# Performance work log

Hardware: AMD Instinct MI355X
Metric: run time of the kernel (lower is better)

## Reference

```python
import jax, jax.numpy as jnp
import numpy as np
import math

D_MODEL = 2048
NUM_HEADS = 16
HEAD_DIM = D_MODEL // NUM_HEADS  # 128
B, S = 2, 2048


def setup_inputs() -> dict:
    key = jax.random.key(0)
    ks = jax.random.split(key, 11)
    s_in = 1.0 / math.sqrt(D_MODEL)
    return {
        "query": jax.random.normal(ks[0], (B, S, D_MODEL), dtype=jnp.float32),
        "key": jax.random.normal(ks[1], (B, S, D_MODEL), dtype=jnp.float32),
        "value": jax.random.normal(ks[2], (B, S, D_MODEL), dtype=jnp.float32),
        "Wq": jax.random.normal(ks[3], (D_MODEL, D_MODEL), dtype=jnp.float32) * s_in,
        "bq": jnp.zeros((D_MODEL,), dtype=jnp.float32),
        "Wk": jax.random.normal(ks[4], (D_MODEL, HEAD_DIM), dtype=jnp.float32) * s_in,
        "bk": jnp.zeros((HEAD_DIM,), dtype=jnp.float32),
        "Wv": jax.random.normal(ks[5], (D_MODEL, HEAD_DIM), dtype=jnp.float32) * s_in,
        "bv": jnp.zeros((HEAD_DIM,), dtype=jnp.float32),
        "Wo": jax.random.normal(ks[6], (D_MODEL, D_MODEL), dtype=jnp.float32) * s_in,
        "bo": jnp.zeros((D_MODEL,), dtype=jnp.float32),
    }


def reference(query, key, value, Wq, bq, Wk, bk, Wv, bv, Wo, bo):
    b, s, d_model = query.shape
    h, d = NUM_HEADS, HEAD_DIM
    # Projections: Q has h heads, K/V have a single shared head (MQA)
    Q = (query @ Wq + bq).reshape(b, s, h, d).transpose(0, 2, 1, 3)  # [b,h,s,d]
    K = key @ Wk + bk      # [b,s,d]
    V = value @ Wv + bv    # [b,s,d]
    scale = 1.0 / math.sqrt(d)
    # broadcast single K head over all h query heads
    scores = jnp.einsum('bhqd,bkd->bhqk', Q, K) * scale  # [b,h,s,s]
    weights = jax.nn.softmax(scores, axis=-1)
    attn = jnp.einsum('bhqk,bkd->bhqd', weights, V)      # [b,h,s,d]
    attn = attn.transpose(0, 2, 1, 3).reshape(b, s, d_model)
    return attn @ Wo + bo
```

## Files before the change

### kernel.cpp

```cpp
#include <hip/hip_runtime.h>


typedef unsigned short u16;
typedef __attribute__((ext_vector_type(8))) short bf16x8;
typedef __attribute__((ext_vector_type(4))) short bf16x4;
typedef __attribute__((ext_vector_type(4))) float f32x4;

#define D_MODEL 2048
#define SEQ     2048
#define NH      16
#define HD      128
#define BK      32

__device__ __forceinline__ u16 f2bf(float f){
  union { float f; unsigned u; } v; v.f = f;
  unsigned r = (v.u + 0x7FFFu + ((v.u >> 16) & 1u)) >> 16;
  return (u16)r;
}

#if __has_builtin(__builtin_amdgcn_cvt_pk_bf16_f32)
__device__ __forceinline__ unsigned pack2bf(float a, float b){
  auto v = __builtin_amdgcn_cvt_pk_bf16_f32(a, b);
  unsigned u; __builtin_memcpy(&u, &v, 4); return u;
}
#else
__device__ __forceinline__ unsigned pack2bf(float a, float b){
  return (unsigned)f2bf(a) | ((unsigned)f2bf(b) << 16);
}
#endif

__device__ __forceinline__ void gll16(const void* g, void* l){
  __builtin_amdgcn_global_load_lds(
      (const __attribute__((address_space(1))) void*)g,
      (__attribute__((address_space(3))) void*)l, 16, 0, 0);
}

__global__ __launch_bounds__(256) void convert3_kernel(
    const float4* __restrict__ a, const float4* __restrict__ b, const float4* __restrict__ c,
    ushort4* __restrict__ oa, ushort4* __restrict__ ob, ushort4* __restrict__ oc){
  int i = blockIdx.x*256 + threadIdx.x;
  float4 va = a[i], vb = b[i], vc = c[i];
  ushort4 ra, rb, rc;
  ra.x=f2bf(va.x); ra.y=f2bf(va.y); ra.z=f2bf(va.z); ra.w=f2bf(va.w);
  rb.x=f2bf(vb.x); rb.y=f2bf(vb.y); rb.z=f2bf(vb.z); rb.w=f2bf(vb.w);
  rc.x=f2bf(vc.x); rc.y=f2bf(vc.y); rc.z=f2bf(vc.z); rc.w=f2bf(vc.w);
  oa[i]=ra; ob[i]=rb; oc[i]=rc;
}

__global__ __launch_bounds__(256) void transpose_all(
    const float* __restrict__ Wq, const float* __restrict__ Wo,
    const float* __restrict__ Wk, const float* __restrict__ Wv,
    u16* __restrict__ WqT, u16* __restrict__ WoT,
    u16* __restrict__ WkT, u16* __restrict__ WvT){
  __shared__ float tt[32][33];
  int id = blockIdx.x;
  const float* in; u16* outp; int C, bx, by;
  if (id < 4096)      { in=Wq; outp=WqT; C=2048; bx=id&63;        by=id>>6; }
  else if (id < 8192) { id-=4096; in=Wo; outp=WoT; C=2048; bx=id&63; by=id>>6; }
  else if (id < 8448) { id-=8192; in=Wk; outp=WkT; C=128;  bx=id&3;  by=id>>2; }
  else                { id-=8448; in=Wv; outp=WvT; C=128;  bx=id&3;  by=id>>2; }
  const int R = 2048;
  int c0 = bx*32, r0 = by*32;
  int tx = threadIdx.x & 31, ty = threadIdx.x >> 5;
  #pragma unroll
  for (int k=0;k<4;k++) tt[ty+k*8][tx] = in[(size_t)(r0+ty+k*8)*C + c0+tx];
  __syncthreads();
  #pragma unroll
  for (int k=0;k<4;k++) outp[(size_t)(c0+ty+k*8)*R + r0+tx] = f2bf(tt[tx][ty+k*8]);
}

__device__ __forceinline__ void gemm_core_db(
    const u16* __restrict__ A, const u16* __restrict__ BT,
    int lda, int ldb, int m0, int n0, int kbeg, int kend,
    u16* As, u16* Bs, f32x4 acc[4][4])
{
  const int t = threadIdx.x;
  const int w = t >> 6, l = t & 63;
  const int wr = w >> 1, wc = w & 1;
  const int c16 = l & 15, q = l >> 4;
  const int srow = l >> 2;
  const int sc   = ((l & 3) ^ ((l >> 3) & 3)) * 8;

  int aoff[4], boff[4];
  #pragma unroll
  for (int mt=0;mt<4;mt++){
    int row = wr*64 + mt*16 + c16;
    aoff[mt] = row*BK + ((q ^ ((row>>1)&3))*8);
  }
  #pragma unroll
  for (int nt=0;nt<4;nt++){
    int row = wc*64 + nt*16 + c16;
    boff[nt] = row*BK + ((q ^ ((row>>1)&3))*8);
  }

  auto issue = [&](int k0, int buf){
    u16* Ad = As + buf*4096;
    u16* Bd = Bs + buf*4096;
    #pragma unroll
    for (int half=0; half<2; half++){
      int r = half*64 + w*16 + srow;
      gll16(A  + (size_t)(m0+r)*lda + k0 + sc, Ad + (half*64 + w*16)*BK);
      gll16(BT + (size_t)(n0+r)*ldb + k0 + sc, Bd + (half*64 + w*16)*BK);
    }
  };

  const int n = (kend - kbeg) / BK;
  issue(kbeg, 0);
  for (int i = 0; i < n; i++){
    __syncthreads();
    if (i+1 < n) issue(kbeg + (i+1)*BK, (i+1)&1);
    const u16* Ab = As + (i&1)*4096;
    const u16* Bb = Bs + (i&1)*4096;
    bf16x8 af[4], bfr[4];
    #pragma unroll
    for (int mt=0;mt<4;mt++) af[mt]  = *(const bf16x8*)(Ab + aoff[mt]);
    #pragma unroll
    for (int nt=0;nt<4;nt++) bfr[nt] = *(const bf16x8*)(Bb + boff[nt]);
    #pragma unroll
    for (int mt=0;mt<4;mt++)
      #pragma unroll
      for (int nt=0;nt<4;nt++)
        acc[mt][nt] = __builtin_amdgcn_mfma_f32_16x16x32_bf16(af[mt], bfr[nt], acc[mt][nt], 0,0,0);
  }
}

__global__ __launch_bounds__(256) void proj_kernel(
    const u16* __restrict__ qb, const u16* __restrict__ kb, const u16* __restrict__ vb,
    const u16* __restrict__ WqT, const u16* __restrict__ WkT, const u16* __restrict__ WvT,
    const float* __restrict__ bq, u16* __restrict__ Qp, float* __restrict__ part)
{
  __shared__ u16 As[2*4096], Bs[2*4096];
  f32x4 acc[4][4];
  f32x4 z = {0.f,0.f,0.f,0.f};
  #pragma unroll
  for (int i=0;i<4;i++) for (int j=0;j<4;j++) acc[i][j] = z;
  const int t = threadIdx.x, w = t>>6, l = t&63, wr = w>>1, wc = w&1, c16 = l&15, q = l>>4;
  int id = blockIdx.x;
  if (id < 512){
    int m0 = (id & 31)*128, n0 = (id >> 5)*128;
    gemm_core_db(qb, WqT, 2048, 2048, m0, n0, 0, 2048, As, Bs, acc);
    #pragma unroll
    for (int mt=0;mt<4;mt++)
      #pragma unroll
      for (int nt=0;nt<4;nt++){
        int col = n0 + wc*64 + nt*16 + c16;
        float bv = bq[col];
        #pragma unroll
        for (int r=0;r<4;r++){
          int row = m0 + wr*64 + mt*16 + q*4 + r;
          Qp[(size_t)row*D_MODEL + col] = f2bf(acc[mt][nt][r] + bv);
        }
      }
  } else {
    int kvid = id - 512;
    int zi = kvid & 3, nb = (kvid >> 2) & 1, mi = kvid >> 3;
    const u16* Am = nb ? vb  : kb;
    const u16* Bm = nb ? WvT : WkT;
    gemm_core_db(Am, Bm, 2048, 2048, mi*128, 0, zi*512, zi*512+512, As, Bs, acc);
    float* dst = part + (size_t)(zi*2 + nb)*524288;
    #pragma unroll
    for (int mt=0;mt<4;mt++)
      #pragma unroll
      for (int nt=0;nt<4;nt++){
        int col = wc*64 + nt*16 + c16;
        #pragma unroll
        for (int r=0;r<4;r++){
          int row = mi*128 + wr*64 + mt*16 + q*4 + r;
          dst[(size_t)row*128 + col] = acc[mt][nt][r];
        }
      }
  }
}

__global__ __launch_bounds__(256) void oproj_kernel(
    const u16* __restrict__ A, const u16* __restrict__ BT, const float* __restrict__ bias,
    float* __restrict__ C)
{
  __shared__ u16 As[2*4096], Bs[2*4096];
  f32x4 acc[4][4];
  f32x4 z = {0.f,0.f,0.f,0.f};
  #pragma unroll
  for (int i=0;i<4;i++) for (int j=0;j<4;j++) acc[i][j] = z;
  int m0 = blockIdx.x*128, n0 = blockIdx.y*128;
  gemm_core_db(A, BT, 2048, 2048, m0, n0, 0, 2048, As, Bs, acc);
  const int t = threadIdx.x, w = t>>6, l = t&63, wr = w>>1, wc = w&1, c16 = l&15, q = l>>4;
  #pragma unroll
  for (int mt=0;mt<4;mt++)
    #pragma unroll
    for (int nt=0;nt<4;nt++){
      int col = n0 + wc*64 + nt*16 + c16;
      float bv = bias[col];
      #pragma unroll
      for (int r=0;r<4;r++){
        int row = m0 + wr*64 + mt*16 + q*4 + r;
        C[(size_t)row*D_MODEL + col] = acc[mt][nt][r] + bv;
      }
    }
}

__global__ __launch_bounds__(256) void kv_reduce_kernel(
    const float* __restrict__ part, const float* __restrict__ bk, const float* __restrict__ bv,
    u16* __restrict__ Kp, u16* __restrict__ VpT){
  int idx = blockIdx.x*256 + threadIdx.x;
  int d = idx & 127, sg = idx >> 7;
  float ka = 0.f, va = 0.f;
  #pragma unroll
  for (int zi=0; zi<4; zi++){
    ka += part[(size_t)(zi*2+0)*524288 + idx];
    va += part[(size_t)(zi*2+1)*524288 + idx];
  }
  Kp[idx] = f2bf(ka + bk[d]);
  int b = sg >> 11, sl = sg & 2047;
  VpT[(size_t)b*262144 + (size_t)d*2048 + sl] = f2bf(va + bv[d]);
}

__global__ __launch_bounds__(512, 4) void attn_kernel(
    const u16* __restrict__ Qp, const u16* __restrict__ Kp,
    const u16* __restrict__ VpT, u16* __restrict__ attnb){
  __shared__ u16 lds[32768];
  u16* Ks = lds;
  u16* Vs = lds + 16384;
  const int t = threadIdx.x;
  const int w = t >> 6, l = t & 63;
  const int c16 = l & 15, q = l >> 4;

  const int qt = blockIdx.x;
  const int bh = blockIdx.y;
  const int b = bh >> 4, h = bh & 15;

  const u16* Qbase = Qp  + ((size_t)(b*SEQ + qt*128 + w*16))*D_MODEL + h*HD;
  const u16* Kbase = Kp  + (size_t)(b*SEQ)*HD;
  const u16* Vbase = VpT + (size_t)b*HD*SEQ;

  {
    u16* qtmp = Vs + w*2048;
    #pragma unroll
    for (int j=0;j<4;j++){
      int r = j*4 + (l >> 4);
      int g = (l & 15) ^ (r & 15);
      gll16(Qbase + (size_t)r*D_MODEL + g*8, qtmp + j*512);
    }
  }
  #pragma unroll
  for (int j=0;j<4;j++){
    int r = j*32 + w*4 + (l >> 4);
    int g = (l & 15) ^ (r & 15);
    gll16(Kbase + (size_t)r*HD + g*8, Ks + j*4096 + w*512);
  }
  __syncthreads();
  bf16x8 qf[4];
  #pragma unroll
  for (int kk=0;kk<4;kk++){
    int ch = kk*4 + q;
    qf[kk] = *(const bf16x8*)(Vs + w*2048 + c16*128 + ((ch ^ c16) & 15)*8);
  }
  __syncthreads();

  f32x4 o[8];
  f32x4 z4 = {0.f,0.f,0.f,0.f};
  #pragma unroll
  for (int dt=0;dt<8;dt++) o[dt] = z4;
  float mrow = -1e30f, lrow = 0.f;
  const float cs = 0.08838834764831845f * 1.4426950408889634f;

  for (int kt = 0; kt < 16; kt++){
    #pragma unroll
    for (int j=0;j<4;j++){
      int d = j*32 + w*4 + (l >> 4);
      int g = (l & 15) ^ (d & 15);
      gll16(Vbase + (size_t)d*SEQ + kt*128 + g*8, Vs + j*4096 + w*512);
    }

    f32x4 s[8];
    #pragma unroll
    for (int kt8=0;kt8<8;kt8++) s[kt8] = z4;
    __builtin_amdgcn_s_setprio(1);
    #pragma unroll
    for (int kt8=0; kt8<8; kt8++){
      #pragma unroll
      for (int kk=0;kk<4;kk++){
        int ch = kk*4 + q;
        bf16x8 kf = *(const bf16x8*)(Ks + (kt8*16 + c16)*128 + ((ch ^ c16) & 15)*8);
        s[kt8] = __builtin_amdgcn_mfma_f32_16x16x32_bf16(kf, qf[kk], s[kt8], 0,0,0);
      }
    }
    __builtin_amdgcn_s_setprio(0);

    float x[8];
    #pragma unroll
    for (int kt8=0;kt8<8;kt8++)
      x[kt8] = fmaxf(fmaxf(s[kt8][0],s[kt8][1]), fmaxf(s[kt8][2],s[kt8][3]));
    float vmax = fmaxf(fmaxf(fmaxf(x[0],x[1]),fmaxf(x[2],x[3])),
                       fmaxf(fmaxf(x[4],x[5]),fmaxf(x[6],x[7])));
    vmax = fmaxf(vmax, __shfl_xor(vmax, 16));
    vmax = fmaxf(vmax, __shfl_xor(vmax, 32));
    float mnew = fmaxf(mrow, vmax);
    float alpha = exp2f((mrow - mnew)*cs);
    float mc = mnew*cs;
    float rs[8];
    #pragma unroll
    for (int kt8=0;kt8<8;kt8++){
      float p0 = exp2f(__builtin_fmaf(s[kt8][0], cs, -mc));
      float p1 = exp2f(__builtin_fmaf(s[kt8][1], cs, -mc));
      float p2 = exp2f(__builtin_fmaf(s[kt8][2], cs, -mc));
      float p3 = exp2f(__builtin_fmaf(s[kt8][3], cs, -mc));
      s[kt8][0]=p0; s[kt8][1]=p1; s[kt8][2]=p2; s[kt8][3]=p3;
      rs[kt8] = (p0+p1)+(p2+p3);
    }
    float rsum = ((rs[0]+rs[1])+(rs[2]+rs[3])) + ((rs[4]+rs[5])+(rs[6]+rs[7]));
    rsum += __shfl_xor(rsum, 16);
    rsum += __shfl_xor(rsum, 32);
    lrow = lrow*alpha + rsum;
    mrow = mnew;

    unsigned long long allone = __ballot(alpha == 1.f);
    if (allone != ~0ull){
      #pragma unroll
      for (int dt=0;dt<8;dt++)
        #pragma unroll
        for (int r=0;r<4;r++) o[dt][r] *= alpha;
    }

    union PU { unsigned u[4]; bf16x8 v; } P32[4];
    #pragma unroll
    for (int kb=0;kb<4;kb++){
      P32[kb].u[0] = pack2bf(s[2*kb][0],   s[2*kb][1]);
      P32[kb].u[1] = pack2bf(s[2*kb][2],   s[2*kb][3]);
      P32[kb].u[2] = pack2bf(s[2*kb+1][0], s[2*kb+1][1]);
      P32[kb].u[3] = pack2bf(s[2*kb+1][2], s[2*kb+1][3]);
    }

    __syncthreads();

    if (kt < 15){
      #pragma unroll
      for (int j=0;j<4;j++){
        int r = j*32 + w*4 + (l >> 4);
        int g = (l & 15) ^ (r & 15);
        gll16(Kbase + (size_t)((kt+1)*128 + r)*HD + g*8, Ks + j*4096 + w*512);
      }
    }

    __builtin_amdgcn_s_setprio(1);
    #pragma unroll
    for (int kb=0; kb<4; kb++){
      int ca = 4*kb + (q>>1);
      int cb = ca + 2;
      #pragma unroll
      for (int dt=0; dt<8; dt++){
        int d = dt*16 + c16;
        union VU { bf16x4 h[2]; bf16x8 v; } vf;
        vf.h[0] = *(const bf16x4*)(Vs + d*128 + ((ca ^ c16) & 15)*8 + (q&1)*4);
        vf.h[1] = *(const bf16x4*)(Vs + d*128 + ((cb ^ c16) & 15)*8 + (q&1)*4);
        o[dt] = __builtin_amdgcn_mfma_f32_16x16x32_bf16(vf.v, P32[kb].v, o[dt], 0,0,0);
      }
    }
    __builtin_amdgcn_s_setprio(0);
    __syncthreads();
  }

  float inv = 1.f / lrow;
  int qrow = qt*128 + w*16 + c16;
  u16* dst = attnb + ((size_t)(b*SEQ) + qrow)*D_MODEL + h*HD + q*4;
  #pragma unroll
  for (int dt=0;dt<8;dt++){
    ushort4 pk;
    pk.x = f2bf(o[dt][0]*inv);
    pk.y = f2bf(o[dt][1]*inv);
    pk.z = f2bf(o[dt][2]*inv);
    pk.w = f2bf(o[dt][3]*inv);
    *(ushort4*)(dst + dt*16) = pk;
  }
}

extern "C" void kernel_launch(void* const* d_in, const int* in_sizes, int n_in,
                              void* d_out, int out_size, void* d_ws, size_t ws_size,
                              hipStream_t stream) {
  (void)in_sizes; (void)n_in; (void)out_size; (void)ws_size;
  const float* query = (const float*)d_in[0];
  const float* key   = (const float*)d_in[1];
  const float* value = (const float*)d_in[2];
  const float* Wq    = (const float*)d_in[3];
  const float* bq    = (const float*)d_in[4];
  const float* Wk    = (const float*)d_in[5];
  const float* bk    = (const float*)d_in[6];
  const float* Wv    = (const float*)d_in[7];
  const float* bv    = (const float*)d_in[8];
  const float* Wo    = (const float*)d_in[9];
  const float* bo    = (const float*)d_in[10];
  float* out = (float*)d_out;

  char* W = (char*)d_ws;
  u16*  qb     = (u16*) (W + 0);
  u16*  kb     = (u16*) (W + 16777216);
  u16*  vb     = (u16*) (W + 33554432);
  u16*  WqT    = (u16*) (W + 50331648);
  u16*  WoT    = (u16*) (W + 58720256);
  u16*  WkT    = (u16*) (W + 67108864);
  u16*  WvT    = (u16*) (W + 67633152);
  u16*  Qp     = (u16*) (W + 68157440);
  u16*  Kp     = (u16*) (W + 84934656);
  u16*  VpT    = (u16*) (W + 85983232);
  u16*  attnb  = (u16*) (W + 87031808);
  float* kvpart= (float*)(W + 103809024);

  convert3_kernel<<<8192, 256, 0, stream>>>(
      (const float4*)query, (const float4*)key, (const float4*)value,
      (ushort4*)qb, (ushort4*)kb, (ushort4*)vb);
  transpose_all<<<8704, 256, 0, stream>>>(Wq, Wo, Wk, Wv, WqT, WoT, WkT, WvT);
  proj_kernel<<<768, 256, 0, stream>>>(qb, kb, vb, WqT, WkT, WvT, bq, Qp, kvpart);
  kv_reduce_kernel<<<2048, 256, 0, stream>>>(kvpart, bk, bv, Kp, VpT);
  attn_kernel<<<dim3(16,32), 512, 0, stream>>>(Qp, Kp, VpT, attnb);
  oproj_kernel<<<dim3(32,16), 256, 0, stream>>>(attnb, WoT, bo, out);
}
```

Before: 432.4 us.

## Process two query subtiles per wave to reuse K/V fragments in attention

Measured after the change: 410.6 us. -5.0%, faster.

```diff
diff --git a/kernel.cpp b/kernel.cpp
--- a/kernel.cpp
+++ b/kernel.cpp
@@ -214,7 +214,7 @@
   VpT[(size_t)b*262144 + (size_t)d*2048 + sl] = f2bf(va + bv[d]);
 }
 
-__global__ __launch_bounds__(512, 4) void attn_kernel(
+__global__ __launch_bounds__(512, 2) void attn_kernel(
     const u16* __restrict__ Qp, const u16* __restrict__ Kp,
     const u16* __restrict__ VpT, u16* __restrict__ attnb){
   __shared__ u16 lds[32768];
@@ -228,39 +228,30 @@
   const int bh = blockIdx.y;
   const int b = bh >> 4, h = bh & 15;
 
-  const u16* Qbase = Qp  + ((size_t)(b*SEQ + qt*128 + w*16))*D_MODEL + h*HD;
+  const u16* Qbase = Qp  + ((size_t)(b*SEQ + qt*256 + w*32))*D_MODEL + h*HD;
   const u16* Kbase = Kp  + (size_t)(b*SEQ)*HD;
   const u16* Vbase = VpT + (size_t)b*HD*SEQ;
 
-  {
-    u16* qtmp = Vs + w*2048;
-    #pragma unroll
-    for (int j=0;j<4;j++){
-      int r = j*4 + (l >> 4);
-      int g = (l & 15) ^ (r & 15);
-      gll16(Qbase + (size_t)r*D_MODEL + g*8, qtmp + j*512);
-    }
-  }
   #pragma unroll
   for (int j=0;j<4;j++){
     int r = j*32 + w*4 + (l >> 4);
     int g = (l & 15) ^ (r & 15);
     gll16(Kbase + (size_t)r*HD + g*8, Ks + j*4096 + w*512);
   }
+  bf16x8 qf[2][4];
+  #pragma unroll
+  for (int qs=0;qs<2;qs++)
+    #pragma unroll
+    for (int kk=0;kk<4;kk++)
+      qf[qs][kk] = *(const bf16x8*)(Qbase + (size_t)(qs*16 + c16)*D_MODEL + (kk*4 + q)*8);
   __syncthreads();
-  bf16x8 qf[4];
-  #pragma unroll
-  for (int kk=0;kk<4;kk++){
-    int ch = kk*4 + q;
-    qf[kk] = *(const bf16x8*)(Vs + w*2048 + c16*128 + ((ch ^ c16) & 15)*8);
-  }
-  __syncthreads();
-
-  f32x4 o[8];
+
+  f32x4 o[2][8];
   f32x4 z4 = {0.f,0.f,0.f,0.f};
   #pragma unroll
-  for (int dt=0;dt<8;dt++) o[dt] = z4;
-  float mrow = -1e30f, lrow = 0.f;
+  for (int qs=0;qs<2;qs++) for (int dt=0;dt<8;dt++) o[qs][dt] = z4;
+  float mrow[2] = {-1e30f, -1e30f};
+  float lrow[2] = {0.f, 0.f};
   const float cs = 0.08838834764831845f * 1.4426950408889634f;
 
   for (int kt = 0; kt < 16; kt++){
@@ -271,9 +262,9 @@
       gll16(Vbase + (size_t)d*SEQ + kt*128 + g*8, Vs + j*4096 + w*512);
     }
 
-    f32x4 s[8];
-    #pragma unroll
-    for (int kt8=0;kt8<8;kt8++) s[kt8] = z4;
+    f32x4 s[2][8];
+    #pragma unroll
+    for (int qs=0;qs<2;qs++) for (int kt8=0;kt8<8;kt8++) s[qs][kt8] = z4;
     __builtin_amdgcn_s_setprio(1);
     #pragma unroll
     for (int kt8=0; kt8<8; kt8++){
@@ -281,54 +272,63 @@
       for (int kk=0;kk<4;kk++){
         int ch = kk*4 + q;
         bf16x8 kf = *(const bf16x8*)(Ks + (kt8*16 + c16)*128 + ((ch ^ c16) & 15)*8);
-        s[kt8] = __builtin_amdgcn_mfma_f32_16x16x32_bf16(kf, qf[kk], s[kt8], 0,0,0);
+        s[0][kt8] = __builtin_amdgcn_mfma_f32_16x16x32_bf16(kf, qf[0][kk], s[0][kt8], 0,0,0);
+        s[1][kt8] = __builtin_amdgcn_mfma_f32_16x16x32_bf16(kf, qf[1][kk], s[1][kt8], 0,0,0);
       }
     }
     __builtin_amdgcn_s_setprio(0);
 
-    float x[8];
-    #pragma unroll
-    for (int kt8=0;kt8<8;kt8++)
-      x[kt8] = fmaxf(fmaxf(s[kt8][0],s[kt8][1]), fmaxf(s[kt8][2],s[kt8][3]));
-    float vmax = fmaxf(fmaxf(fmaxf(x[0],x[1]),fmaxf(x[2],x[3])),
-                       fmaxf(fmaxf(x[4],x[5]),fmaxf(x[6],x[7])));
-    vmax = fmaxf(vmax, __shfl_xor(vmax, 16));
-    vmax = fmaxf(vmax, __shfl_xor(vmax, 32));
-    float mnew = fmaxf(mrow, vmax);
-    float alpha = exp2f((mrow - mnew)*cs);
-    float mc = mnew*cs;
-    float rs[8];
-    #pragma unroll
-    for (int kt8=0;kt8<8;kt8++){
-      float p0 = exp2f(__builtin_fmaf(s[kt8][0], cs, -mc));
-      float p1 = exp2f(__builtin_fmaf(s[kt8][1], cs, -mc));
-      float p2 = exp2f(__builtin_fmaf(s[kt8][2], cs, -mc));
-      float p3 = exp2f(__builtin_fmaf(s[kt8][3], cs, -mc));
-      s[kt8][0]=p0; s[kt8][1]=p1; s[kt8][2]=p2; s[kt8][3]=p3;
-      rs[kt8] = (p0+p1)+(p2+p3);
-    }
-    float rsum = ((rs[0]+rs[1])+(rs[2]+rs[3])) + ((rs[4]+rs[5])+(rs[6]+rs[7]));
-    rsum += __shfl_xor(rsum, 16);
-    rsum += __shfl_xor(rsum, 32);
-    lrow = lrow*alpha + rsum;
-    mrow = mnew;
-
-    unsigned long long allone = __ballot(alpha == 1.f);
+    float alpha[2];
+    #pragma unroll
+    for (int qs=0; qs<2; qs++){
+      float x[8];
+      #pragma unroll
+      for (int kt8=0;kt8<8;kt8++)
+        x[kt8] = fmaxf(fmaxf(s[qs][kt8][0],s[qs][kt8][1]), fmaxf(s[qs][kt8][2],s[qs][kt8][3]));
+      float vmax = fmaxf(fmaxf(fmaxf(x[0],x[1]),fmaxf(x[2],x[3])),
+                         fmaxf(fmaxf(x[4],x[5]),fmaxf(x[6],x[7])));
+      vmax = fmaxf(vmax, __shfl_xor(vmax, 16));
+      vmax = fmaxf(vmax, __shfl_xor(vmax, 32));
+      float mnew = fmaxf(mrow[qs], vmax);
+      alpha[qs] = exp2f((mrow[qs] - mnew)*cs);
+      float mc = mnew*cs;
+      float rs[8];
+      #pragma unroll
+      for (int kt8=0;kt8<8;kt8++){
+        float p0 = exp2f(__builtin_fmaf(s[qs][kt8][0], cs, -mc));
+        float p1 = exp2f(__builtin_fmaf(s[qs][kt8][1], cs, -mc));
+        float p2 = exp2f(__builtin_fmaf(s[qs][kt8][2], cs, -mc));
+        float p3 = exp2f(__builtin_fmaf(s[qs][kt8][3], cs, -mc));
+        s[qs][kt8][0]=p0; s[qs][kt8][1]=p1; s[qs][kt8][2]=p2; s[qs][kt8][3]=p3;
+        rs[kt8] = (p0+p1)+(p2+p3);
+      }
+      float rsum = ((rs[0]+rs[1])+(rs[2]+rs[3])) + ((rs[4]+rs[5])+(rs[6]+rs[7]));
+      rsum += __shfl_xor(rsum, 16);
+      rsum += __shfl_xor(rsum, 32);
+      lrow[qs] = lrow[qs]*alpha[qs] + rsum;
+      mrow[qs] = mnew;
+    }
+
+    unsigned long long allone = __ballot(alpha[0] == 1.f && alpha[1] == 1.f);
     if (allone != ~0ull){
       #pragma unroll
-      for (int dt=0;dt<8;dt++)
+      for (int qs=0;qs<2;qs++)
         #pragma unroll
-        for (int r=0;r<4;r++) o[dt][r] *= alpha;
-    }
-
-    union PU { unsigned u[4]; bf16x8 v; } P32[4];
-    #pragma unroll
-    for (int kb=0;kb<4;kb++){
-      P32[kb].u[0] = pack2bf(s[2*kb][0],   s[2*kb][1]);
-      P32[kb].u[1] = pack2bf(s[2*kb][2],   s[2*kb][3]);
-      P32[kb].u[2] = pack2bf(s[2*kb+1][0], s[2*kb+1][1]);
-      P32[kb].u[3] = pack2bf(s[2*kb+1][2], s[2*kb+1][3]);
-    }
+        for (int dt=0;dt<8;dt++)
+          #pragma unroll
+          for (int r=0;r<4;r++) o[qs][dt][r] *= alpha[qs];
+    }
+
+    union PU { unsigned u[4]; bf16x8 v; } P32[2][4];
+    #pragma unroll
+    for (int qs=0;qs<2;qs++)
+      #pragma unroll
+      for (int kb=0;kb<4;kb++){
+        P32[qs][kb].u[0] = pack2bf(s[qs][2*kb][0],   s[qs][2*kb][1]);
+        P32[qs][kb].u[1] = pack2bf(s[qs][2*kb][2],   s[qs][2*kb][3]);
+        P32[qs][kb].u[2] = pack2bf(s[qs][2*kb+1][0], s[qs][2*kb+1][1]);
+        P32[qs][kb].u[3] = pack2bf(s[qs][2*kb+1][2], s[qs][2*kb+1][3]);
+      }
 
     __syncthreads();
 
@@ -352,24 +352,28 @@
         union VU { bf16x4 h[2]; bf16x8 v; } vf;
         vf.h[0] = *(const bf16x4*)(Vs + d*128 + ((ca ^ c16) & 15)*8 + (q&1)*4);
         vf.h[1] = *(const bf16x4*)(Vs + d*128 + ((cb ^ c16) & 15)*8 + (q&1)*4);
-        o[dt] = __builtin_amdgcn_mfma_f32_16x16x32_bf16(vf.v, P32[kb].v, o[dt], 0,0,0);
+        o[0][dt] = __builtin_amdgcn_mfma_f32_16x16x32_bf16(vf.v, P32[0][kb].v, o[0][dt], 0,0,0);
+        o[1][dt] = __builtin_amdgcn_mfma_f32_16x16x32_bf16(vf.v, P32[1][kb].v, o[1][dt], 0,0,0);
       }
     }
     __builtin_amdgcn_s_setprio(0);
     __syncthreads();
   }
 
-  float inv = 1.f / lrow;
-  int qrow = qt*128 + w*16 + c16;
-  u16* dst = attnb + ((size_t)(b*SEQ) + qrow)*D_MODEL + h*HD + q*4;
-  #pragma unroll
-  for (int dt=0;dt<8;dt++){
-    ushort4 pk;
-    pk.x = f2bf(o[dt][0]*inv);
-    pk.y = f2bf(o[dt][1]*inv);
-    pk.z = f2bf(o[dt][2]*inv);
-    pk.w = f2bf(o[dt][3]*inv);
-    *(ushort4*)(dst + dt*16) = pk;
+  #pragma unroll
+  for (int qs=0;qs<2;qs++){
+    float inv = 1.f / lrow[qs];
+    int qrow = qt*256 + w*32 + qs*16 + c16;
+    u16* dst = attnb + ((size_t)(b*SEQ) + qrow)*D_MODEL + h*HD + q*4;
+    #pragma unroll
+    for (int dt=0;dt<8;dt++){
+      ushort4 pk;
+      pk.x = f2bf(o[qs][dt][0]*inv);
+      pk.y = f2bf(o[qs][dt][1]*inv);
+      pk.z = f2bf(o[qs][dt][2]*inv);
+      pk.w = f2bf(o[qs][dt][3]*inv);
+      *(ushort4*)(dst + dt*16) = pk;
+    }
   }
 }
 
@@ -410,6 +414,6 @@
   transpose_all<<<8704, 256, 0, stream>>>(Wq, Wo, Wk, Wv, WqT, WoT, WkT, WvT);
   proj_kernel<<<768, 256, 0, stream>>>(qb, kb, vb, WqT, WkT, WvT, bq, Qp, kvpart);
   kv_reduce_kernel<<<2048, 256, 0, stream>>>(kvpart, bk, bv, Kp, VpT);
-  attn_kernel<<<dim3(16,32), 512, 0, stream>>>(Qp, Kp, VpT, attnb);
+  attn_kernel<<<dim3(8,32), 512, 0, stream>>>(Qp, Kp, VpT, attnb);
   oproj_kernel<<<dim3(32,16), 256, 0, stream>>>(attnb, WoT, bo, out);
 }
```
